# Kernel optimization log

Measured on AMD Instinct MI355X. Metric: run time of the kernel, lower is better.

The kernel has to match this reference:

```python
import jax, jax.numpy as jnp
import numpy as np

N = 50000      # num_nodes
E = 800000     # num_edges
D = 128        # hidden_dim
POOL_RATIO = 0.5
CROSS_W = 1.0  # cross_weight


def _gcn(x, W, b, src, dst, n):
    """GCNConv: symmetric-normalized aggregation with self-loops. Dropout is identity (eval)."""
    loops = jnp.arange(n)
    s = jnp.concatenate([src, loops])
    d = jnp.concatenate([dst, loops])
    deg = jax.ops.segment_sum(jnp.ones(s.shape, x.dtype), d, num_segments=n)
    inv_sqrt = jax.lax.rsqrt(jnp.maximum(deg, 1.0))  # deg >= 1 due to self-loops
    xw = x @ W                                        # [n, D]
    msg = xw[s] * (inv_sqrt[s] * inv_sqrt[d])[:, None]  # [E+n, D] gather
    return jax.ops.segment_sum(msg, d, num_segments=n) + b


def _prelu(x, a):
    return jnp.where(x >= 0, x, a * x)


def setup_inputs() -> dict:
    key = jax.random.key(0)
    ks = jax.random.split(key, 8)
    glorot = lambda k, sh: jax.random.normal(k, sh, jnp.float32) * np.float32(np.sqrt(2.0 / (sh[0] + sh[1])))
    return {
        "feat": jax.random.normal(ks[0], (N, D), jnp.float32),
        "h_neg": jax.random.normal(ks[1], (N, D), jnp.float32),
        "edge_index": jax.random.randint(ks[2], (2, E), 0, N),
        "Wd": glorot(ks[3], (D, D)),
        "bd": jnp.zeros((D,), jnp.float32),
        "prelu_a": jnp.full((1,), 0.25, jnp.float32),
        "Wbil": glorot(ks[4], (D, D)),
        "bbil": jnp.zeros((1,), jnp.float32),
        "Wg1": glorot(ks[5], (D, D)),
        "bg1": jnp.zeros((D,), jnp.float32),
        "Wg2": glorot(ks[6], (D, D)),
        "bg2": jnp.zeros((D,), jnp.float32),
        "Wg3": glorot(ks[7], (D, D)),
        "bg3": jnp.zeros((D,), jnp.float32),
    }


def reference(feat, h_neg, edge_index, Wd, bd, prelu_a, Wbil, bbil,
              Wg1, bg1, Wg2, bg2, Wg3, bg3):
    src, dst = edge_index[0], edge_index[1]
    # --- IndexSelect: dense layer on pos/neg features ---
    h_pos = _prelu(feat @ Wd + bd, prelu_a)
    h_neg_d = _prelu(h_neg @ Wd + bd, prelu_a)
    embed = _gcn(h_pos, Wg1, bg1, src, dst, N)
    h_center = jax.nn.sigmoid(embed)
    # Discriminator (bilinear) positive scores -> node importance
    score_pos = jnp.einsum('nd,de,ne->n', h_pos, Wbil, h_center) + bbil[0]
    _ = jnp.einsum('nd,de,ne->n', h_neg_d, Wbil, h_center) + bbil[0]  # score_neg (logits branch)
    scores = jax.nn.sigmoid(score_pos)
    order = jnp.argsort(-scores)           # descending
    k = int(POOL_RATIO * N)
    select_idx = order[:k]
    select_scores = scores[order][:k]
    # --- GraphPool (use_gcn=True): down-sample GCN, gather, scale ---
    pooled = _gcn(embed, Wg2, bg2, src, dst, N)[select_idx] * select_scores[:, None]
    # --- GraphUnpool: scatter into zeros, up-sample GCN ---
    fine = jnp.zeros((N, D), feat.dtype).at[select_idx].set(pooled)
    out = _gcn(fine, Wg3, bg3, src, dst, N)
    # --- cross/fuse connection ---
    return out + CROSS_W * embed
```

## Files before the change

### kernel.cpp

```cpp
#include <hip/hip_runtime.h>
#include <hip/hip_bf16.h>

#define NN 50000
#define NE 800000
#define DD 128
#define KSEL 25000
#define NBK 391
#define NBLKA 98
#define AB 12500

typedef unsigned int uint32;
typedef unsigned short ushort16;
typedef __attribute__((ext_vector_type(8))) short bf16x8;
typedef __attribute__((ext_vector_type(4))) float f32x4;

__device__ __forceinline__ float sigmoidf(float x){ return 1.f/(1.f+__expf(-x)); }

__device__ __forceinline__ unsigned short f2b(float f){
  union{float f; unsigned u;} v; v.f=f;
  unsigned r=(v.u + 0x7fffu + ((v.u>>16)&1u))>>16;
  return (unsigned short)r;
}

__device__ __forceinline__ void addbf2(float&lo,float&hi,uint32 u,float w){
  lo+=__uint_as_float(u<<16)*w;
  hi+=__uint_as_float(u&0xffff0000u)*w;
}

__global__ __launch_bounds__(256) void k_prep(const float* __restrict__ Wbil,
    float* __restrict__ WbT, const float* __restrict__ Wg2, ushort16* __restrict__ Wt2b,
    const float* __restrict__ Wg3, ushort16* __restrict__ Wt3b,
    int* __restrict__ zspan, int* __restrict__ btot){
  int i=blockIdx.x*256+threadIdx.x;
  if(i<DD*DD){
    int n=i>>7, k=i&127;
    WbT[i]=Wbil[k*DD+n];
    Wt2b[i]=f2b(Wg2[(size_t)k*DD+n]);
    Wt3b[i]=f2b(Wg3[(size_t)k*DD+n]);
  }
  if(i<8512) zspan[i]=0;
  if(i<NBK) btot[i]=0;
}

__global__ __launch_bounds__(1024) void k_bcount(const int* __restrict__ dst,
    int* __restrict__ btot, int* __restrict__ blkcnt){
  __shared__ int h[NBK];
  int tid=threadIdx.x;
  for(int i=tid;i<NBK;i+=1024) h[i]=0;
  __syncthreads();
  int e0=blockIdx.x*8192;
  #pragma unroll
  for(int t=0;t<8;t++){
    int e=e0+t*1024+tid;
    if(e<NE) atomicAdd(&h[dst[e]>>7],1);
  }
  __syncthreads();
  for(int i=tid;i<NBK;i+=1024){
    int c=h[i];
    blkcnt[blockIdx.x*NBK+i]=c;
    if(c) atomicAdd(&btot[i],c);
  }
}

__global__ __launch_bounds__(512) void k_bscan(const int* __restrict__ btot,
    int* __restrict__ boff, const int* __restrict__ blkcnt, int* __restrict__ blkbase,
    int* __restrict__ row_start){
  __shared__ int sdata[512];
  int tid=threadIdx.x;
  int v=(tid<NBK)?btot[tid]:0;
  sdata[tid]=v; __syncthreads();
  for(int off=1;off<512;off<<=1){
    int y=(tid>=off)?sdata[tid-off]:0;
    __syncthreads();
    sdata[tid]+=y;
    __syncthreads();
  }
  int excl=sdata[tid]-v;
  if(tid<NBK) boff[tid]=excl;
  if(tid==NBK-1){ boff[NBK]=excl+v; row_start[NN]=NE; }
  if(tid<NBK){
    int run=excl;
    for(int b=0;b<NBLKA;b++){
      int c=blkcnt[b*NBK+tid];
      blkbase[b*NBK+tid]=run;
      run+=c;
    }
  }
}

__global__ __launch_bounds__(1024) void k_bscatter(const int* __restrict__ src,
    const int* __restrict__ dst, const int* __restrict__ blkbase, uint32* __restrict__ pairs){
  __shared__ int cur[NBK];
  int tid=threadIdx.x;
  for(int i=tid;i<NBK;i+=1024) cur[i]=blkbase[blockIdx.x*NBK+i];
  __syncthreads();
  int e0=blockIdx.x*8192;
  #pragma unroll
  for(int t=0;t<8;t++){
    int e=e0+t*1024+tid;
    if(e<NE){
      int d=dst[e];
      int p=atomicAdd(&cur[d>>7],1);
      pairs[p]=(unsigned)src[e] | ((unsigned)(d&127)<<17);
    }
  }
}

__global__ __launch_bounds__(256) void k_bfinal(const uint32* __restrict__ pairs,
    const int* __restrict__ boff, int* __restrict__ row_start,
    float* __restrict__ inv_sq, int* __restrict__ csr_src){
  __shared__ int degl[128];
  __shared__ int cur[128];
  __shared__ int ssum[2];
  int b=blockIdx.x, tid=threadIdx.x;
  int lo=boff[b], hi=boff[b+1];
  if(tid<128) degl[tid]=0;
  __syncthreads();
  for(int e=lo+tid;e<hi;e+=256) atomicAdd(&degl[pairs[e]>>17],1);
  __syncthreads();
  int v=0,x=0;
  if(tid<128){
    v=degl[tid]; x=v;
    #pragma unroll
    for(int off=1;off<64;off<<=1){
      int y=__shfl_up(x,off,64);
      if((tid&63)>=off) x+=y;
    }
    if((tid&63)==63) ssum[tid>>6]=x;
  }
  __syncthreads();
  if(tid<128){
    int incl=x+((tid>=64)?ssum[0]:0);
    int node=b*128+tid;
    int excl=lo+incl-v;
    if(node<NN){
      row_start[node]=excl;
      cur[tid]=excl;
      inv_sq[node]=1.f/sqrtf((float)(v+1));
    }
  }
  __syncthreads();
  for(int e=lo+tid;e<hi;e+=256){
    uint32 u=pairs[e];
    int p=atomicAdd(&cur[u>>17],1);
    csr_src[p]=(int)(u&0x1FFFFu);
  }
}

template<int IN_SIG,int ACT,int FUSE_SCORE>
__global__ __launch_bounds__(256) void k_gemm64t(const float* __restrict__ A,
    const float* __restrict__ W, const float* __restrict__ bias,
    float* __restrict__ outf,
    const float* __restrict__ aparam, const float* __restrict__ hp,
    const float* __restrict__ bbil, float* __restrict__ score){
  __shared__ float Al[64][132];
  int tid=threadIdx.x;
  int row0=blockIdx.x*64;
  {
    const float4* A4=(const float4*)(A+(size_t)row0*DD);
    #pragma unroll
    for(int i=0;i<8;i++){
      int idx=i*256+tid;
      int r=idx>>5, c=(idx&31)*4;
      float4 v=make_float4(0.f,0.f,0.f,0.f);
      if(row0+r<NN) v=A4[idx];
      if(IN_SIG){ v.x=sigmoidf(v.x); v.y=sigmoidf(v.y); v.z=sigmoidf(v.z); v.w=sigmoidf(v.w); }
      *(float4*)&Al[r][c]=v;
    }
  }
  __syncthreads();
  int tx=tid&15, ty=tid>>4;
  float acc[4][8];
  #pragma unroll
  for(int i=0;i<4;i++)
    #pragma unroll
    for(int c=0;c<8;c++) acc[i][c]=0.f;

  for(int k=0;k<DD;k+=4){
    float wv[4][8];
    #pragma unroll
    for(int r=0;r<4;r++){
      float4 lo=*(const float4*)&W[(size_t)(k+r)*DD+tx*8];
      float4 hi=*(const float4*)&W[(size_t)(k+r)*DD+tx*8+4];
      wv[r][0]=lo.x; wv[r][1]=lo.y; wv[r][2]=lo.z; wv[r][3]=lo.w;
      wv[r][4]=hi.x; wv[r][5]=hi.y; wv[r][6]=hi.z; wv[r][7]=hi.w;
    }
    #pragma unroll
    for(int i=0;i<4;i++){
      float4 a=*(const float4*)&Al[ty+16*i][k];
      #pragma unroll
      for(int c=0;c<8;c++)
        acc[i][c]+=a.x*wv[0][c]+a.y*wv[1][c]+a.z*wv[2][c]+a.w*wv[3][c];
    }
  }

  if(FUSE_SCORE){
    float bb=bbil[0];
    #pragma unroll
    for(int i=0;i<4;i++){
      int r=row0+ty+16*i;
      float p=0.f;
      if(r<NN){
        float4 h0=*(const float4*)&hp[(size_t)r*DD+tx*8];
        float4 h1=*(const float4*)&hp[(size_t)r*DD+tx*8+4];
        p=acc[i][0]*h0.x+acc[i][1]*h0.y+acc[i][2]*h0.z+acc[i][3]*h0.w
         +acc[i][4]*h1.x+acc[i][5]*h1.y+acc[i][6]*h1.z+acc[i][7]*h1.w;
      }
      p+=__shfl_xor(p,1,64); p+=__shfl_xor(p,2,64);
      p+=__shfl_xor(p,4,64); p+=__shfl_xor(p,8,64);
      if(tx==0 && r<NN) score[r]=sigmoidf(p+bb);
    }
    return;
  }
  float bl[8]={0,0,0,0,0,0,0,0};
  if(bias){
    float4 b0=*(const float4*)&bias[tx*8];
    float4 b1=*(const float4*)&bias[tx*8+4];
    bl[0]=b0.x; bl[1]=b0.y; bl[2]=b0.z; bl[3]=b0.w;
    bl[4]=b1.x; bl[5]=b1.y; bl[6]=b1.z; bl[7]=b1.w;
  }
  float ap=ACT?aparam[0]:0.f;
  #pragma unroll
  for(int i=0;i<4;i++){
    int r=row0+ty+16*i;
    if(r<NN){
      float o[8];
      #pragma unroll
      for(int c=0;c<8;c++){
        float t=acc[i][c]+bl[c];
        if(ACT) t=t>=0.f?t:ap*t;
        o[c]=t;
      }
      float4 q0; q0.x=o[0]; q0.y=o[1]; q0.z=o[2]; q0.w=o[3];
      float4 q1; q1.x=o[4]; q1.y=o[5]; q1.z=o[6]; q1.w=o[7];
      *(float4*)&outf[(size_t)r*DD+tx*8]=q0;
      *(float4*)&outf[(size_t)r*DD+tx*8+4]=q1;
    }
  }
}

template<int ROWLIST>
__global__ __launch_bounds__(256) void k_gemm_mfma(const float* __restrict__ A,
    const ushort16* __restrict__ Wtb, ushort16* __restrict__ outb,
    const int* __restrict__ rlist){
  __shared__ __align__(16) unsigned short Asl[64][136];
  __shared__ __align__(16) unsigned short Wsl[128][136];
  int tid=threadIdx.x;
  int row0=blockIdx.x*64;
  {
    const uint4* Wg=(const uint4*)Wtb;
    #pragma unroll
    for(int i=0;i<8;i++){
      int idx=i*256+tid;
      int n=idx>>4, k8=(idx&15)*8;
      uint4 v=Wg[idx];
      *(uint4*)&Wsl[n][k8]=v;
    }
  }
  {
    #pragma unroll
    for(int i=0;i<8;i++){
      int idx=i*256+tid;
      int r=idx>>5, c=(idx&31)*4;
      int gr; bool ok;
      if(ROWLIST){ int ri=row0+r; ok=(ri<KSEL); gr=ok?rlist[ri]:0; }
      else { gr=row0+r; ok=(gr<NN); }
      float4 v=make_float4(0.f,0.f,0.f,0.f);
      if(ok) v=*(const float4*)&A[(size_t)gr*DD+c];
      ushort4 pk;
      pk.x=f2b(v.x); pk.y=f2b(v.y); pk.z=f2b(v.z); pk.w=f2b(v.w);
      *(ushort4*)&Asl[r][c]=pk;
    }
  }
  __syncthreads();
  int lane=tid&63, w=tid>>6;
  int lr=lane&15, lk=lane>>4;
  f32x4 acc[8];
  #pragma unroll
  for(int nf=0;nf<8;nf++){ acc[nf][0]=0.f; acc[nf][1]=0.f; acc[nf][2]=0.f; acc[nf][3]=0.f; }
  #pragma unroll
  for(int kk=0;kk<4;kk++){
    int k0=kk*32+lk*8;
    bf16x8 a=*(bf16x8*)&Asl[w*16+lr][k0];
    #pragma unroll
    for(int nf=0;nf<8;nf++){
      bf16x8 b=*(bf16x8*)&Wsl[nf*16+lr][k0];
      acc[nf]=__builtin_amdgcn_mfma_f32_16x16x32_bf16(a,b,acc[nf],0,0,0);
    }
  }
  int orow[4]; bool ok[4];
  #pragma unroll
  for(int i=0;i<4;i++){
    int ri=row0+w*16+lk*4+i;
    if(ROWLIST){ ok[i]=(ri<KSEL); orow[i]=ok[i]?rlist[ri]:0; }
    else { orow[i]=ri; ok[i]=(ri<NN); }
  }
  #pragma unroll
  for(int nf=0;nf<8;nf++){
    int col=nf*16+lr;
    #pragma unroll
    for(int i=0;i<4;i++){
      if(ok[i]) outb[(size_t)orow[i]*DD+col]=f2b(acc[nf][i]);
    }
  }
}

__global__ __launch_bounds__(256) void k_agg_f32(const float* __restrict__ xw,
    const int* __restrict__ row_start, const int* __restrict__ csr,
    const float* __restrict__ inv, const float* __restrict__ bias,
    float* __restrict__ outp){
  int node=blockIdx.x*4+(threadIdx.x>>6);
  if(node>=NN) return;
  int lane=threadIdx.x&63;
  int g=lane>>5, li=lane&31;
  int rs=row_start[node], re=row_start[node+1];
  float a0=0.f,a1=0.f,a2=0.f,a3=0.f;
  int j=rs;
  for(; j+7<re; j+=8){
    int s0=csr[j+g], s1=csr[j+2+g], s2=csr[j+4+g], s3=csr[j+6+g];
    float w0=inv[s0], w1=inv[s1], w2=inv[s2], w3=inv[s3];
    float4 v0=*(const float4*)&xw[(size_t)s0*DD+li*4];
    float4 v1=*(const float4*)&xw[(size_t)s1*DD+li*4];
    float4 v2=*(const float4*)&xw[(size_t)s2*DD+li*4];
    float4 v3=*(const float4*)&xw[(size_t)s3*DD+li*4];
    a0+=v0.x*w0+v1.x*w1+v2.x*w2+v3.x*w3;
    a1+=v0.y*w0+v1.y*w1+v2.y*w2+v3.y*w3;
    a2+=v0.z*w0+v1.z*w1+v2.z*w2+v3.z*w3;
    a3+=v0.w*w0+v1.w*w1+v2.w*w2+v3.w*w3;
  }
  for(; j+1<re; j+=2){
    int s=csr[j+g];
    float w=inv[s];
    float4 v=*(const float4*)&xw[(size_t)s*DD+li*4];
    a0+=v.x*w; a1+=v.y*w; a2+=v.z*w; a3+=v.w*w;
  }
  if(j<re && g==0){
    int s=csr[j]; float w=inv[s];
    float4 v=*(const float4*)&xw[(size_t)s*DD+li*4];
    a0+=v.x*w; a1+=v.y*w; a2+=v.z*w; a3+=v.w*w;
  }
  if(g==0){
    float wd=inv[node];
    float4 v=*(const float4*)&xw[(size_t)node*DD+li*4];
    a0+=v.x*wd; a1+=v.y*wd; a2+=v.z*wd; a3+=v.w*wd;
  }
  a0+=__shfl_xor(a0,32,64); a1+=__shfl_xor(a1,32,64);
  a2+=__shfl_xor(a2,32,64); a3+=__shfl_xor(a3,32,64);
  if(g==0){
    float wn=inv[node];
    float4 bv=*(const float4*)&bias[li*4];
    float4 o;
    o.x=a0*wn+bv.x; o.y=a1*wn+bv.y; o.z=a2*wn+bv.z; o.w=a3*wn+bv.w;
    *(float4*)&outp[(size_t)node*DD+li*4]=o;
  }
}

template<int MODE>
__global__ __launch_bounds__(256) void k_agg_b16(const uint32* __restrict__ xwb,
    const int* __restrict__ row_start, const int* __restrict__ csr,
    const float* __restrict__ inv, const float* __restrict__ bias,
    float* __restrict__ outp, const float* __restrict__ score,
    const unsigned char* __restrict__ sel, const float* __restrict__ addbuf,
    const int* __restrict__ list){
  int idx4=blockIdx.x*4+(threadIdx.x>>6);
  int node;
  if(MODE==1){ if(idx4>=KSEL) return; node=list[idx4]; }
  else { node=idx4; if(node>=NN) return; }
  int lane=threadIdx.x&63;
  int g=lane>>4, li=lane&15;
  int rs=row_start[node], re=row_start[node+1];
  float a[8];
  #pragma unroll
  for(int c=0;c<8;c++) a[c]=0.f;
  int j=rs;
  for(; j+7<re; j+=8){
    int sA=csr[j+g], sB=csr[j+4+g];
    if(MODE!=2 || sel[sA]){
      float w=inv[sA];
      uint4 u=*(const uint4*)(xwb+(size_t)sA*64+li*4);
      addbf2(a[0],a[1],u.x,w); addbf2(a[2],a[3],u.y,w);
      addbf2(a[4],a[5],u.z,w); addbf2(a[6],a[7],u.w,w);
    }
    if(MODE!=2 || sel[sB]){
      float w=inv[sB];
      uint4 u=*(const uint4*)(xwb+(size_t)sB*64+li*4);
      addbf2(a[0],a[1],u.x,w); addbf2(a[2],a[3],u.y,w);
      addbf2(a[4],a[5],u.z,w); addbf2(a[6],a[7],u.w,w);
    }
  }
  for(; j+3<re; j+=4){
    int s=csr[j+g];
    if(MODE!=2 || sel[s]){
      float w=inv[s];
      uint4 u=*(const uint4*)(xwb+(size_t)s*64+li*4);
      addbf2(a[0],a[1],u.x,w); addbf2(a[2],a[3],u.y,w);
      addbf2(a[4],a[5],u.z,w); addbf2(a[6],a[7],u.w,w);
    }
  }
  int rem=re-j;
  if(g<rem){
    int s=csr[j+g];
    if(MODE!=2 || sel[s]){
      float w=inv[s];
      uint4 u=*(const uint4*)(xwb+(size_t)s*64+li*4);
      addbf2(a[0],a[1],u.x,w); addbf2(a[2],a[3],u.y,w);
      addbf2(a[4],a[5],u.z,w); addbf2(a[6],a[7],u.w,w);
    }
  }
  if(g==0 && (MODE!=2 || sel[node])){
    float wd=inv[node];
    uint4 u=*(const uint4*)(xwb+(size_t)node*64+li*4);
    addbf2(a[0],a[1],u.x,wd); addbf2(a[2],a[3],u.y,wd);
    addbf2(a[4],a[5],u.z,wd); addbf2(a[6],a[7],u.w,wd);
  }
  #pragma unroll
  for(int c=0;c<8;c++){
    a[c]+=__shfl_xor(a[c],16,64);
    a[c]+=__shfl_xor(a[c],32,64);
  }
  if(g<2){
    float wn=inv[node];
    int cb=li*8+g*4;
    float4 bv=*(const float4*)&bias[cb];
    float r0=a[g*4+0]*wn+bv.x, r1=a[g*4+1]*wn+bv.y;
    float r2=a[g*4+2]*wn+bv.z, r3=a[g*4+3]*wn+bv.w;
    if(MODE==1){
      float sc=score[node];
      r0*=sc; r1*=sc; r2*=sc; r3*=sc;
    } else {
      float4 ad=*(const float4*)&addbuf[(size_t)node*DD+cb];
      r0+=ad.x; r1+=ad.y; r2+=ad.z; r3+=ad.w;
    }
    float4 o; o.x=r0; o.y=r1; o.z=r2; o.w=r3;
    *(float4*)&outp[(size_t)node*DD+cb]=o;
  }
}

template<int NB,int PASS>
__global__ __launch_bounds__(256) void k_hist(const float* __restrict__ score,
    int* __restrict__ ghist, const int* __restrict__ ctrl){
  __shared__ int lh[NB];
  int tid=threadIdx.x;
  for(int i=tid;i<NB;i+=256) lh[i]=0;
  __syncthreads();
  int p0=0,p01=0;
  if(PASS==1) p0=ctrl[0];
  if(PASS==2) p01=ctrl[2];
  for(int i=blockIdx.x*256+tid; i<NN; i+=gridDim.x*256){
    unsigned b=__float_as_uint(score[i]);
    if(PASS==0) atomicAdd(&lh[b>>20],1);
    else if(PASS==1){ if((int)(b>>20)==p0) atomicAdd(&lh[(b>>8)&0xFFF],1); }
    else { if((int)(b>>8)==p01) atomicAdd(&lh[b&0xFF],1); }
  }
  __syncthreads();
  for(int i=tid;i<NB;i+=256){ int v=lh[i]; if(v) atomicAdd(&ghist[i],v); }
}

template<int NB,int PASS>
__global__ void k_findb(const int* __restrict__ hist, int* __restrict__ ctrl){
  const int NT=NB/4;
  __shared__ int gsum[NT];
  int t=threadIdx.x;
  int s=hist[t*4]+hist[t*4+1]+hist[t*4+2]+hist[t*4+3];
  int x=s; gsum[t]=x; __syncthreads();
  for(int off=1;off<NT;off<<=1){
    int y=(t+off<NT)?gsum[t+off]:0;
    __syncthreads();
    x+=y; gsum[t]=x; __syncthreads();
  }
  int base;
  if(PASS==0) base=0; else if(PASS==1) base=ctrl[1]; else base=ctrl[3];
  int above=base+((t<NT-1)?gsum[t+1]:0);
  int incl=base+gsum[t];
  if(above<KSEL && incl>=KSEL){
    int c=above, B=0;
    for(int b=3;b>=0;b--){
      int hb=hist[t*4+b];
      if(c+hb>=KSEL){ B=t*4+b; break; }
      c+=hb;
    }
    if(PASS==0){ ctrl[0]=B; ctrl[1]=c; }
    else if(PASS==1){ ctrl[2]=(ctrl[0]<<12)|B; ctrl[3]=c; }
    else { ctrl[4]=(int)((((unsigned)ctrl[2])<<8)|(unsigned)B); ctrl[5]=KSEL-c; }
  }
}

__global__ void k_sel(const float* __restrict__ score, int* __restrict__ ctrl,
                      int* __restrict__ tie_list, unsigned char* __restrict__ sel,
                      int* __restrict__ list){
  int i=blockIdx.x*256+threadIdx.x;
  if(i>=NN) return;
  unsigned b=__float_as_uint(score[i]);
  unsigned thr=(unsigned)ctrl[4];
  if(b>thr){
    sel[i]=1;
    int p=atomicAdd(&ctrl[7],1);
    list[p]=i;
  }
  else if(b==thr){
    sel[i]=0;
    int p=atomicAdd(&ctrl[6],1);
    if(p<4096) tie_list[p]=i;
  } else sel[i]=0;
}

__global__ __launch_bounds__(256) void k_tie(const int* __restrict__ ctrl_c,
    int* __restrict__ ctrl, const int* __restrict__ tie_list,
    unsigned char* __restrict__ sel, int* __restrict__ list){
  int m=ctrl_c[6]; if(m>4096) m=4096;
  int needed=ctrl_c[5];
  for(int t=threadIdx.x; t<m; t+=blockDim.x){
    int idx=tie_list[t];
    int rank=0;
    for(int j=0;j<m;j++) rank+=(tie_list[j]<idx)?1:0;
    if(rank<needed){
      sel[idx]=1;
      int p=atomicAdd(&ctrl[7],1);
      list[p]=idx;
    }
  }
}

extern "C" void kernel_launch(void* const* d_in, const int* in_sizes, int n_in,
                              void* d_out, int out_size, void* d_ws, size_t ws_size,
                              hipStream_t stream){
  const float* feat   =(const float*)d_in[0];
  const int*   ei     =(const int*)  d_in[2];
  const int*   src    = ei;
  const int*   dst    = ei + NE;
  const float* Wd     =(const float*)d_in[3];
  const float* bd     =(const float*)d_in[4];
  const float* prelu_a=(const float*)d_in[5];
  const float* Wbil   =(const float*)d_in[6];
  const float* bbil   =(const float*)d_in[7];
  const float* Wg1    =(const float*)d_in[8];
  const float* bg1    =(const float*)d_in[9];
  const float* Wg2    =(const float*)d_in[10];
  const float* bg2    =(const float*)d_in[11];
  const float* Wg3    =(const float*)d_in[12];
  const float* bg3    =(const float*)d_in[13];
  float* out=(float*)d_out;

  char* p=(char*)d_ws;
  auto alloc=[&](size_t bytes)->void*{ void* r=(void*)p; p+=((bytes+255)/256)*256; return r; };
  float* h_pos   =(float*)alloc((size_t)NN*DD*4);
  float* embed   =(float*)alloc((size_t)NN*DD*4);
  float* xw      =(float*)alloc((size_t)NN*DD*4);
  float* score   =(float*)alloc((size_t)NN*4);
  float* inv_sq  =(float*)alloc((size_t)NN*4);
  float* WbT     =(float*)alloc((size_t)DD*DD*4);
  ushort16* Wt2b =(ushort16*)alloc((size_t)DD*DD*2);
  ushort16* Wt3b =(ushort16*)alloc((size_t)DD*DD*2);
  int*   row_st  =(int*)  alloc((size_t)(NN+1)*4);
  int*   csr_src =(int*)  alloc((size_t)NE*4);
  int*   ctrl    =(int*)  alloc(64);
  int*   hist0   =(int*)  alloc(4096*4);
  int*   hist1   =(int*)  alloc(4096*4);
  int*   hist2   =(int*)  alloc(256*4);
  int*   tie_list=(int*)  alloc(4096*4);
  int*   list    =(int*)  alloc((size_t)KSEL*4);
  unsigned char* sel=(unsigned char*)alloc(NN);
  int*   btot    =(int*)  alloc((size_t)NBK*4);
  int*   boff    =(int*)  alloc((size_t)(NBK+1)*4);
  int*   blkcnt  =(int*)  alloc((size_t)NBLKA*NBK*4);
  int*   blkbase =(int*)  alloc((size_t)NBLKA*NBK*4);
  uint32* pairs  =(uint32*)xw;
  ushort16* xwb  =(ushort16*)xw;
  float* fine = out;

  const int NB=(NN+255)/256;
  const int GB=(NN+63)/64;
  const int GBL=(KSEL+63)/64;
  const int ABL=(KSEL+3)/4;

  k_prep<<<64,256,0,stream>>>(Wbil, WbT, Wg2, Wt2b, Wg3, Wt3b, ctrl, btot);

  k_bcount  <<<NBLKA,1024,0,stream>>>(dst, btot, blkcnt);
  k_bscan   <<<1,512,0,stream>>>(btot, boff, blkcnt, blkbase, row_st);
  k_bscatter<<<NBLKA,1024,0,stream>>>(src, dst, blkbase, pairs);
  k_bfinal  <<<NBK,256,0,stream>>>(pairs, boff, row_st, inv_sq, csr_src);

  k_gemm64t<0,1,0><<<GB,256,0,stream>>>(feat, Wd, bd, h_pos, prelu_a, nullptr, nullptr, nullptr);
  k_gemm64t<0,0,0><<<GB,256,0,stream>>>(h_pos, Wg1, nullptr, xw, nullptr, nullptr, nullptr, nullptr);
  k_agg_f32<<<AB,256,0,stream>>>(xw, row_st, csr_src, inv_sq, bg1, embed);
  k_gemm64t<1,0,1><<<GB,256,0,stream>>>(embed, WbT, nullptr, nullptr, nullptr, h_pos, bbil, score);
  k_hist<4096,0><<<64,256,0,stream>>>(score, hist0, ctrl);
  k_findb<4096,0><<<1,1024,0,stream>>>(hist0, ctrl);
  k_hist<4096,1><<<64,256,0,stream>>>(score, hist1, ctrl);
  k_findb<4096,1><<<1,1024,0,stream>>>(hist1, ctrl);
  k_hist<256,2><<<64,256,0,stream>>>(score, hist2, ctrl);
  k_findb<256,2><<<1,64,0,stream>>>(hist2, ctrl);
  k_sel<<<NB,256,0,stream>>>(score, ctrl, tie_list, sel, list);
  k_tie<<<1,256,0,stream>>>(ctrl, ctrl, tie_list, sel, list);
  k_gemm_mfma<0><<<GB,256,0,stream>>>(embed, Wt2b, xwb, nullptr);
  k_agg_b16<1><<<ABL,256,0,stream>>>((const uint32*)xwb, row_st, csr_src, inv_sq, bg2, fine, score, sel, nullptr, list);
  k_gemm_mfma<1><<<GBL,256,0,stream>>>(fine, Wt3b, xwb, list);
  k_agg_b16<2><<<AB,256,0,stream>>>((const uint32*)xwb, row_st, csr_src, inv_sq, bg3, out, nullptr, sel, embed, nullptr);
}
```

Baseline: 334.7 us.

## Fuse threshold-finding and tie-resolution into last-block epilogues; remap fp32 GEMM threads

Removes four small single-block launches (three k_findb and k_tie). Their work now runs in the last block to finish k_hist and k_sel, detected with an atomic completion counter in ctrl, and the ctrl buffer is enlarged to hold those counters. Separately, the fp32 tiled GEMM changes its thread mapping from 16x16 threads with 4x8 outputs each to 32x8 threads with 8x4 outputs each, and the score reduction is adjusted to match. The intent is to cut launch and serialization overhead in the top-k selection chain. The risks are threadfence-based ordering, and the counters at ctrl[8..11] may not be zeroed if k_prep only clears a fixed range.

```diff
diff --git a/kernel.cpp b/kernel.cpp
--- a/kernel.cpp
+++ b/kernel.cpp
@@ -25,6 +25,10 @@
 __device__ __forceinline__ void addbf2(float&lo,float&hi,uint32 u,float w){
   lo+=__uint_as_float(u<<16)*w;
   hi+=__uint_as_float(u&0xffff0000u)*w;
+}
+
+__device__ __forceinline__ int aload(const int* p){
+  return __hip_atomic_load(p,__ATOMIC_RELAXED,__HIP_MEMORY_SCOPE_AGENT);
 }
 
 __global__ __launch_bounds__(256) void k_prep(const float* __restrict__ Wbil,
@@ -169,72 +173,58 @@
     }
   }
   __syncthreads();
-  int tx=tid&15, ty=tid>>4;
-  float acc[4][8];
-  #pragma unroll
-  for(int i=0;i<4;i++)
-    #pragma unroll
-    for(int c=0;c<8;c++) acc[i][c]=0.f;
+  int tx=tid&31, ty=tid>>5;
+  float acc[8][4];
+  #pragma unroll
+  for(int i=0;i<8;i++)
+    #pragma unroll
+    for(int c=0;c<4;c++) acc[i][c]=0.f;
 
   for(int k=0;k<DD;k+=4){
-    float wv[4][8];
-    #pragma unroll
-    for(int r=0;r<4;r++){
-      float4 lo=*(const float4*)&W[(size_t)(k+r)*DD+tx*8];
-      float4 hi=*(const float4*)&W[(size_t)(k+r)*DD+tx*8+4];
-      wv[r][0]=lo.x; wv[r][1]=lo.y; wv[r][2]=lo.z; wv[r][3]=lo.w;
-      wv[r][4]=hi.x; wv[r][5]=hi.y; wv[r][6]=hi.z; wv[r][7]=hi.w;
-    }
-    #pragma unroll
-    for(int i=0;i<4;i++){
-      float4 a=*(const float4*)&Al[ty+16*i][k];
-      #pragma unroll
-      for(int c=0;c<8;c++)
-        acc[i][c]+=a.x*wv[0][c]+a.y*wv[1][c]+a.z*wv[2][c]+a.w*wv[3][c];
+    float4 wv0=*(const float4*)&W[(size_t)(k+0)*DD+tx*4];
+    float4 wv1=*(const float4*)&W[(size_t)(k+1)*DD+tx*4];
+    float4 wv2=*(const float4*)&W[(size_t)(k+2)*DD+tx*4];
+    float4 wv3=*(const float4*)&W[(size_t)(k+3)*DD+tx*4];
+    #pragma unroll
+    for(int i=0;i<8;i++){
+      float4 a=*(const float4*)&Al[ty+8*i][k];
+      acc[i][0]+=a.x*wv0.x+a.y*wv1.x+a.z*wv2.x+a.w*wv3.x;
+      acc[i][1]+=a.x*wv0.y+a.y*wv1.y+a.z*wv2.y+a.w*wv3.y;
+      acc[i][2]+=a.x*wv0.z+a.y*wv1.z+a.z*wv2.z+a.w*wv3.z;
+      acc[i][3]+=a.x*wv0.w+a.y*wv1.w+a.z*wv2.w+a.w*wv3.w;
     }
   }
 
   if(FUSE_SCORE){
     float bb=bbil[0];
     #pragma unroll
-    for(int i=0;i<4;i++){
-      int r=row0+ty+16*i;
+    for(int i=0;i<8;i++){
+      int r=row0+ty+8*i;
       float p=0.f;
       if(r<NN){
-        float4 h0=*(const float4*)&hp[(size_t)r*DD+tx*8];
-        float4 h1=*(const float4*)&hp[(size_t)r*DD+tx*8+4];
-        p=acc[i][0]*h0.x+acc[i][1]*h0.y+acc[i][2]*h0.z+acc[i][3]*h0.w
-         +acc[i][4]*h1.x+acc[i][5]*h1.y+acc[i][6]*h1.z+acc[i][7]*h1.w;
+        float4 h=*(const float4*)&hp[(size_t)r*DD+tx*4];
+        p=acc[i][0]*h.x+acc[i][1]*h.y+acc[i][2]*h.z+acc[i][3]*h.w;
       }
-      p+=__shfl_xor(p,1,64); p+=__shfl_xor(p,2,64);
-      p+=__shfl_xor(p,4,64); p+=__shfl_xor(p,8,64);
+      p+=__shfl_xor(p,16,64); p+=__shfl_xor(p,8,64);
+      p+=__shfl_xor(p,4,64);  p+=__shfl_xor(p,2,64); p+=__shfl_xor(p,1,64);
       if(tx==0 && r<NN) score[r]=sigmoidf(p+bb);
     }
     return;
   }
-  float bl[8]={0,0,0,0,0,0,0,0};
-  if(bias){
-    float4 b0=*(const float4*)&bias[tx*8];
-    float4 b1=*(const float4*)&bias[tx*8+4];
-    bl[0]=b0.x; bl[1]=b0.y; bl[2]=b0.z; bl[3]=b0.w;
-    bl[4]=b1.x; bl[5]=b1.y; bl[6]=b1.z; bl[7]=b1.w;
-  }
+  float4 bv=make_float4(0.f,0.f,0.f,0.f);
+  if(bias) bv=*(const float4*)&bias[tx*4];
   float ap=ACT?aparam[0]:0.f;
   #pragma unroll
-  for(int i=0;i<4;i++){
-    int r=row0+ty+16*i;
+  for(int i=0;i<8;i++){
+    int r=row0+ty+8*i;
     if(r<NN){
-      float o[8];
-      #pragma unroll
-      for(int c=0;c<8;c++){
-        float t=acc[i][c]+bl[c];
-        if(ACT) t=t>=0.f?t:ap*t;
-        o[c]=t;
+      float4 o;
+      o.x=acc[i][0]+bv.x; o.y=acc[i][1]+bv.y; o.z=acc[i][2]+bv.z; o.w=acc[i][3]+bv.w;
+      if(ACT){
+        o.x=o.x>=0.f?o.x:ap*o.x; o.y=o.y>=0.f?o.y:ap*o.y;
+        o.z=o.z>=0.f?o.z:ap*o.z; o.w=o.w>=0.f?o.w:ap*o.w;
       }
-      float4 q0; q0.x=o[0]; q0.y=o[1]; q0.z=o[2]; q0.w=o[3];
-      float4 q1; q1.x=o[4]; q1.y=o[5]; q1.z=o[6]; q1.w=o[7];
-      *(float4*)&outf[(size_t)r*DD+tx*8]=q0;
-      *(float4*)&outf[(size_t)r*DD+tx*8+4]=q1;
+      *(float4*)&outf[(size_t)r*DD+tx*4]=o;
     }
   }
 }
@@ -438,8 +428,10 @@
 
 template<int NB,int PASS>
 __global__ __launch_bounds__(256) void k_hist(const float* __restrict__ score,
-    int* __restrict__ ghist, const int* __restrict__ ctrl){
+    int* __restrict__ ghist, int* __restrict__ ctrl){
   __shared__ int lh[NB];
+  __shared__ int gs[256];
+  __shared__ int lastf;
   int tid=threadIdx.x;
   for(int i=tid;i<NB;i+=256) lh[i]=0;
   __syncthreads();
@@ -454,29 +446,31 @@
   }
   __syncthreads();
   for(int i=tid;i<NB;i+=256){ int v=lh[i]; if(v) atomicAdd(&ghist[i],v); }
-}
-
-template<int NB,int PASS>
-__global__ void k_findb(const int* __restrict__ hist, int* __restrict__ ctrl){
-  const int NT=NB/4;
-  __shared__ int gsum[NT];
-  int t=threadIdx.x;
-  int s=hist[t*4]+hist[t*4+1]+hist[t*4+2]+hist[t*4+3];
-  int x=s; gsum[t]=x; __syncthreads();
-  for(int off=1;off<NT;off<<=1){
-    int y=(t+off<NT)?gsum[t+off]:0;
-    __syncthreads();
-    x+=y; gsum[t]=x; __syncthreads();
+  __syncthreads();
+  if(tid==0){
+    __threadfence();
+    int v=atomicAdd(&ctrl[8+PASS],1);
+    lastf=(v==(int)gridDim.x-1);
+  }
+  __syncthreads();
+  if(!lastf) return;
+  const int BPT=NB/256;
+  int s=0;
+  #pragma unroll
+  for(int q=0;q<BPT;q++) s+=aload(&ghist[tid*BPT+q]);
+  int x=s; gs[tid]=x; __syncthreads();
+  for(int off=1;off<256;off<<=1){
+    int y=(tid+off<256)?gs[tid+off]:0;
+    __syncthreads(); x+=y; gs[tid]=x; __syncthreads();
   }
   int base;
   if(PASS==0) base=0; else if(PASS==1) base=ctrl[1]; else base=ctrl[3];
-  int above=base+((t<NT-1)?gsum[t+1]:0);
-  int incl=base+gsum[t];
+  int above=base+x-s, incl=base+x;
   if(above<KSEL && incl>=KSEL){
     int c=above, B=0;
-    for(int b=3;b>=0;b--){
-      int hb=hist[t*4+b];
-      if(c+hb>=KSEL){ B=t*4+b; break; }
+    for(int b=BPT-1;b>=0;b--){
+      int hb=aload(&ghist[tid*BPT+b]);
+      if(c+hb>=KSEL){ B=tid*BPT+b; break; }
       c+=hb;
     }
     if(PASS==0){ ctrl[0]=B; ctrl[1]=c; }
@@ -485,34 +479,39 @@
   }
 }
 
-__global__ void k_sel(const float* __restrict__ score, int* __restrict__ ctrl,
-                      int* __restrict__ tie_list, unsigned char* __restrict__ sel,
-                      int* __restrict__ list){
-  int i=blockIdx.x*256+threadIdx.x;
-  if(i>=NN) return;
-  unsigned b=__float_as_uint(score[i]);
-  unsigned thr=(unsigned)ctrl[4];
-  if(b>thr){
-    sel[i]=1;
-    int p=atomicAdd(&ctrl[7],1);
-    list[p]=i;
-  }
-  else if(b==thr){
-    sel[i]=0;
-    int p=atomicAdd(&ctrl[6],1);
-    if(p<4096) tie_list[p]=i;
-  } else sel[i]=0;
-}
-
-__global__ __launch_bounds__(256) void k_tie(const int* __restrict__ ctrl_c,
-    int* __restrict__ ctrl, const int* __restrict__ tie_list,
+__global__ __launch_bounds__(256) void k_sel(const float* __restrict__ score,
+    int* __restrict__ ctrl, int* __restrict__ tie_list,
     unsigned char* __restrict__ sel, int* __restrict__ list){
-  int m=ctrl_c[6]; if(m>4096) m=4096;
-  int needed=ctrl_c[5];
-  for(int t=threadIdx.x; t<m; t+=blockDim.x){
-    int idx=tie_list[t];
+  __shared__ int lastf;
+  int tid=threadIdx.x;
+  int i=blockIdx.x*256+tid;
+  if(i<NN){
+    unsigned b=__float_as_uint(score[i]);
+    unsigned thr=(unsigned)ctrl[4];
+    if(b>thr){
+      sel[i]=1;
+      int p=atomicAdd(&ctrl[7],1);
+      list[p]=i;
+    } else if(b==thr){
+      sel[i]=0;
+      int p=atomicAdd(&ctrl[6],1);
+      if(p<4096) __hip_atomic_store(&tie_list[p],i,__ATOMIC_RELAXED,__HIP_MEMORY_SCOPE_AGENT);
+    } else sel[i]=0;
+  }
+  __syncthreads();
+  if(tid==0){
+    __threadfence();
+    int v=atomicAdd(&ctrl[11],1);
+    lastf=(v==(int)gridDim.x-1);
+  }
+  __syncthreads();
+  if(!lastf) return;
+  int m=aload(&ctrl[6]); if(m>4096) m=4096;
+  int needed=ctrl[5];
+  for(int t=tid;t<m;t+=256){
+    int idx=aload(&tie_list[t]);
     int rank=0;
-    for(int j=0;j<m;j++) rank+=(tie_list[j]<idx)?1:0;
+    for(int j2=0;j2<m;j2++) rank+=(aload(&tie_list[j2])<idx)?1:0;
     if(rank<needed){
       sel[idx]=1;
       int p=atomicAdd(&ctrl[7],1);
@@ -553,7 +552,7 @@
   ushort16* Wt3b =(ushort16*)alloc((size_t)DD*DD*2);
   int*   row_st  =(int*)  alloc((size_t)(NN+1)*4);
   int*   csr_src =(int*)  alloc((size_t)NE*4);
-  int*   ctrl    =(int*)  alloc(64);
+  int*   ctrl    =(int*)  alloc(256);
   int*   hist0   =(int*)  alloc(4096*4);
   int*   hist1   =(int*)  alloc(4096*4);
   int*   hist2   =(int*)  alloc(256*4);
@@ -585,13 +584,9 @@
   k_agg_f32<<<AB,256,0,stream>>>(xw, row_st, csr_src, inv_sq, bg1, embed);
   k_gemm64t<1,0,1><<<GB,256,0,stream>>>(embed, WbT, nullptr, nullptr, nullptr, h_pos, bbil, score);
   k_hist<4096,0><<<64,256,0,stream>>>(score, hist0, ctrl);
-  k_findb<4096,0><<<1,1024,0,stream>>>(hist0, ctrl);
   k_hist<4096,1><<<64,256,0,stream>>>(score, hist1, ctrl);
-  k_findb<4096,1><<<1,1024,0,stream>>>(hist1, ctrl);
   k_hist<256,2><<<64,256,0,stream>>>(score, hist2, ctrl);
-  k_findb<256,2><<<1,64,0,stream>>>(hist2, ctrl);
   k_sel<<<NB,256,0,stream>>>(score, ctrl, tie_list, sel, list);
-  k_tie<<<1,256,0,stream>>>(ctrl, ctrl, tie_list, sel, list);
   k_gemm_mfma<0><<<GB,256,0,stream>>>(embed, Wt2b, xwb, nullptr);
   k_agg_b16<1><<<ABL,256,0,stream>>>((const uint32*)xwb, row_st, csr_src, inv_sq, bg2, fine, score, sel, nullptr, list);
   k_gemm_mfma<1><<<GBL,256,0,stream>>>(fine, Wt3b, xwb, list);
```

Measured after the change: 330.0 us. No clear change (-1.4%).
